# Optimization experiments

Measured on AMD Instinct MI355X. Metric: run time of the kernel, lower is better.

## Reference

```python
import jax, jax.numpy as jnp
import numpy as np

N = 100_000      # nodes
E = 1_600_000    # edges (avg degree 16)
IN, H, OUT = 960, 192, 3
NB = 6           # block_num


def setup_inputs() -> dict:
    key = jax.random.key(0)
    ks = jax.random.split(key, 14)
    s = 0.05  # weight init scale
    x = jax.random.normal(ks[0], (N, IN), jnp.float32)
    src = jax.random.randint(ks[1], (E,), 0, N, jnp.int32)
    dst = jax.random.randint(ks[2], (E,), 0, N, jnp.int32)
    # normalized adjacency values (like D^-1 A entries)
    ew = jax.random.uniform(ks[3], (E,), jnp.float32) / 16.0
    w1 = jax.random.normal(ks[4], (IN, H), jnp.float32) * s
    l1 = jax.random.normal(ks[5], (IN, H), jnp.float32) * s
    b1 = jnp.zeros((H,), jnp.float32)
    wb = jax.random.normal(ks[6], (2 * NB, H, H), jnp.float32) * s
    lb = jax.random.normal(ks[7], (2 * NB, H, H), jnp.float32) * s
    bb = jnp.zeros((2 * NB, H), jnp.float32)
    w2 = jax.random.normal(ks[8], (H, OUT), jnp.float32) * s
    l2 = jax.random.normal(ks[9], (H, OUT), jnp.float32) * s
    b2 = jnp.zeros((OUT,), jnp.float32)
    return dict(x=x, src=src, dst=dst, ew=ew, w1=w1, l1=l1, b1=b1,
                wb=wb, lb=lb, bb=bb, w2=w2, l2=l2, b2=b2)


def reference(x, src, dst, ew, w1, l1, b1, wb, lb, bb, w2, l2, b2):
    def gcn(h, w, lw, b):
        # GraphConvolution: spmm(adj, h @ w) + h @ loop_w + b
        sup = h @ w                                   # [N, F_out]
        msg = sup[src] * ew[:, None]                  # gather + weight  [E, F_out]
        agg = jax.ops.segment_sum(msg, dst, num_segments=N)
        return agg + h @ lw + b

    h = gcn(x, w1, l1, b1)                            # conv1: in_dim -> hidden
    for i in range(NB):                               # GResBlocks
        a = gcn(h, wb[2 * i], lb[2 * i], bb[2 * i])
        a = gcn(a, wb[2 * i + 1], lb[2 * i + 1], bb[2 * i + 1])
        h = (h + a) * 0.5                             # residual scaling
    x_cat = h
    x_out = gcn(x_cat, w2, l2, b2)                    # conv2: hidden -> out_dim
    return (x_out, x_cat)
```

## Files before the change

kernel.cpp:

```cpp
#include <hip/hip_runtime.h>

typedef __attribute__((ext_vector_type(8))) short short8;
typedef __attribute__((ext_vector_type(4))) float f32x4;
typedef __attribute__((ext_vector_type(4))) int int4v;
typedef __attribute__((ext_vector_type(2))) unsigned int u32x2;

__device__ __forceinline__ float bf2f(unsigned short u) {
  return __uint_as_float(((unsigned)u) << 16);
}
__device__ __forceinline__ unsigned short f2bf(float f) {
  unsigned u = __float_as_uint(f);
  return (unsigned short)((u + 0x7FFFu + ((u >> 16) & 1u)) >> 16);
}

#define GLB_CAST(p) ((const __attribute__((address_space(1))) void*)(p))
#define LDS_CAST(p) ((__attribute__((address_space(3))) void*)(p))

__global__ void count_kernel(const int* __restrict__ dst, int* __restrict__ cnt, int E) {
  int e = blockIdx.x * blockDim.x + threadIdx.x;
  if (e < E) atomicAdd(&cnt[dst[e] + 1], 1);
}

__global__ __launch_bounds__(256) void scan_bsum_kernel(const int* __restrict__ cnt,
                                                        int* __restrict__ bsum, int n) {
  __shared__ int buf[256];
  int tid = threadIdx.x;
  int j0 = blockIdx.x * 1024 + tid * 4;
  int s = 0;
#pragma unroll
  for (int k = 0; k < 4; k++) {
    int j = j0 + k;
    if (j < n) s += cnt[j];
  }
  buf[tid] = s;
  __syncthreads();
  for (int off = 128; off > 0; off >>= 1) {
    if (tid < off) buf[tid] += buf[tid + off];
    __syncthreads();
  }
  if (tid == 0) bsum[blockIdx.x] = buf[0];
}

__global__ __launch_bounds__(256) void scan_small_kernel(const int* __restrict__ bsum,
                                                         int* __restrict__ boff, int nb) {
  __shared__ int buf[2][256];
  int tid = threadIdx.x;
  int C = (nb + 255) >> 8;
  int start = tid * C;
  int end = start + C; if (end > nb) end = nb;
  int s = 0;
  for (int j = start; j < end; j++) s += bsum[j];
  buf[0][tid] = s;
  __syncthreads();
  int pin = 0;
  for (int off = 1; off < 256; off <<= 1) {
    int v = buf[pin][tid];
    if (tid >= off) v += buf[pin][tid - off];
    buf[pin ^ 1][tid] = v;
    pin ^= 1;
    __syncthreads();
  }
  int run = (tid == 0) ? 0 : buf[pin][tid - 1];
  for (int j = start; j < end; j++) {
    boff[j] = run;
    run += bsum[j];
  }
}

__global__ __launch_bounds__(256) void scan_final_kernel(const int* __restrict__ cnt,
                                                         const int* __restrict__ boff,
                                                         int* __restrict__ rowptr,
                                                         int* __restrict__ cur,
                                                         int n, int nrows) {
  __shared__ int buf[2][256];
  int tid = threadIdx.x;
  int j0 = blockIdx.x * 1024 + tid * 4;
  int v[4];
  int s = 0;
#pragma unroll
  for (int k = 0; k < 4; k++) {
    int j = j0 + k;
    v[k] = (j < n) ? cnt[j] : 0;
    s += v[k];
  }
  buf[0][tid] = s;
  __syncthreads();
  int pin = 0;
  for (int off = 1; off < 256; off <<= 1) {
    int t = buf[pin][tid];
    if (tid >= off) t += buf[pin][tid - off];
    buf[pin ^ 1][tid] = t;
    pin ^= 1;
    __syncthreads();
  }
  int run = boff[blockIdx.x] + ((tid == 0) ? 0 : buf[pin][tid - 1]);
#pragma unroll
  for (int k = 0; k < 4; k++) {
    int j = j0 + k;
    if (j < n) {
      run += v[k];
      rowptr[j] = run;
      if (j < nrows) cur[j] = run;
    }
  }
}

__global__ void fill_kernel(const int* __restrict__ src, const int* __restrict__ dst,
                            const float* __restrict__ ew,
                            int* __restrict__ cur, int2* __restrict__ s_edge, int E) {
  int e = blockIdx.x * blockDim.x + threadIdx.x;
  if (e >= E) return;
  int r = dst[e];
  int pos = atomicAdd(&cur[r], 1);
  s_edge[pos] = make_int2(src[e], __float_as_int(ew[e]));
}

__global__ void prep_w_kernel(const float* __restrict__ w1,
                              const float* __restrict__ l1,
                              const float* __restrict__ wb,
                              const float* __restrict__ lb,
                              unsigned short* __restrict__ Wt1,
                              unsigned short* __restrict__ Wcatb) {
  int tid = blockIdx.x * blockDim.x + threadIdx.x;
  const int n1 = 30 * 1536 * 8;
  const int nc = 12 * 12 * 768 * 8;
  if (tid < n1) {
    int tile = tid / 12288;
    int r = tid % 12288;
    int slot = r >> 3, e = r & 7;
    int q = slot / 384, c = slot % 384;
    int k = tile * 32 + q * 8 + e;
    Wt1[tid] = f2bf((c < 192) ? w1[k * 192 + c] : l1[k * 192 + (c - 192)]);
  } else if (tid < n1 + nc) {
    int u = tid - n1;
    int i = u / 73728;
    int r = u % 73728;
    int tile = r / 6144;
    int r2 = r % 6144;
    int slot = r2 >> 3, e = r2 & 7;
    int q = slot / 192, c = slot % 192;
    int k = tile * 32 + q * 8 + e;
    Wcatb[u] = f2bf((k < 192) ? wb[((size_t)i * 192 + k) * 192 + c]
                              : lb[((size_t)i * 192 + (k - 192)) * 192 + c]);
  }
}

__device__ __forceinline__ short8 cvt_pair(f32x4 a, f32x4 b) {
  short8 r;
  r[0] = (short)f2bf(a[0]); r[1] = (short)f2bf(a[1]);
  r[2] = (short)f2bf(a[2]); r[3] = (short)f2bf(a[3]);
  r[4] = (short)f2bf(b[0]); r[5] = (short)f2bf(b[1]);
  r[6] = (short)f2bf(b[2]); r[7] = (short)f2bf(b[3]);
  return r;
}

__global__ __launch_bounds__(512) void gemm_f32_kernel(const float* __restrict__ A,
                                                       const unsigned short* __restrict__ Wt,
                                                       unsigned short* __restrict__ out,
                                                       int nrows, int K) {
  __shared__ char lds_raw[40960];

  int tid = threadIdx.x;
  int lane = tid & 63;
  int w = tid >> 6;
  int rg = w >> 1, ch = w & 1;
  int row0blk = blockIdx.x * 256;
  int row0 = row0blk + rg * 64;
  int l15 = lane & 15, lq = lane >> 4;

  f32x4 acc[12][4];
#pragma unroll
  for (int cf = 0; cf < 12; cf++)
#pragma unroll
    for (int rf = 0; rf < 4; rf++) acc[cf][rf] = (f32x4)(0.0f);

  int tiles = K / 32;
  for (int tile = 0; tile < tiles; ++tile) {
    __syncthreads();
#pragma unroll
    for (int it = 0; it < 3; ++it) {
      int slot = it * 512 + tid;
      const unsigned short* g = Wt + ((size_t)tile * 1536 + slot) * 8;
      __builtin_amdgcn_global_load_lds(GLB_CAST(g), LDS_CAST(lds_raw + 16384 + slot * 16), 16, 0, 0);
    }
#pragma unroll
    for (int it = 0; it < 2; ++it) {
      int fs = it * 512 + tid;
      int row = fs >> 2, q8 = fs & 3;
      int grow = row0blk + row;
      if (grow > nrows - 1) grow = nrows - 1;
      const float* g = A + (size_t)grow * K + tile * 32 + q8 * 8;
      f32x4 a0 = *reinterpret_cast<const f32x4*>(g);
      f32x4 a1 = *reinterpret_cast<const f32x4*>(g + 4);
      *reinterpret_cast<short8*>(lds_raw + q8 * 4096 + row * 16) = cvt_pair(a0, a1);
    }
    __syncthreads();

    short8 af[4];
#pragma unroll
    for (int rf = 0; rf < 4; rf++)
      af[rf] = *reinterpret_cast<const short8*>(
          lds_raw + lq * 4096 + (rg * 64 + rf * 16 + l15) * 16);
#pragma unroll
    for (int cf = 0; cf < 12; cf++) {
      const short8 bf = *reinterpret_cast<const short8*>(
          lds_raw + 16384 + (lq * 384 + ch * 192 + cf * 16 + l15) * 16);
#pragma unroll
      for (int rf = 0; rf < 4; rf++)
        acc[cf][rf] = __builtin_amdgcn_mfma_f32_16x16x32_bf16(bf, af[rf], acc[cf][rf], 0, 0, 0);
    }
  }

#pragma unroll
  for (int rf = 0; rf < 4; rf++) {
    int row = row0 + rf * 16 + l15;
    if (row >= nrows) continue;
    unsigned short* orow = out + (size_t)row * 384 + ch * 192 + lq * 4;
#pragma unroll
    for (int cf = 0; cf < 12; cf++) {
      u32x2 pv;
      pv[0] = (unsigned)f2bf(acc[cf][rf][0]) | ((unsigned)f2bf(acc[cf][rf][1]) << 16);
      pv[1] = (unsigned)f2bf(acc[cf][rf][2]) | ((unsigned)f2bf(acc[cf][rf][3]) << 16);
      *reinterpret_cast<u32x2*>(orow + cf * 16) = pv;
    }
  }
}

__global__ __launch_bounds__(256) void spmm_t_kernel(const unsigned short* __restrict__ t,
                                                     const int* __restrict__ rowptr,
                                                     const int2* __restrict__ s_edge,
                                                     const float* __restrict__ bias,
                                                     unsigned short* __restrict__ out16,
                                                     int n) {
  int tid = blockIdx.x * blockDim.x + threadIdx.x;
  int node = tid >> 3;
  int sub = tid & 7;
  if (node >= n) return;
  int co = sub * 8;

  float acc[3][8];
#pragma unroll
  for (int q = 0; q < 3; q++)
#pragma unroll
    for (int j = 0; j < 8; j++) acc[q][j] = 0.0f;

  int e0 = rowptr[node], e1 = rowptr[node + 1];
  int ne = e1 - e0;
  int base = 0;
  for (; base + 8 <= ne; base += 8) {
    int2 rec = s_edge[e0 + base + sub];
#pragma unroll
    for (int half = 0; half < 2; half++) {
      short8 v[4][3];
      float wgt[4];
#pragma unroll
      for (int k = 0; k < 4; k++) {
        int kk = half * 4 + k;
        int sn = __shfl(rec.x, kk, 8);
        wgt[k] = __int_as_float(__shfl(rec.y, kk, 8));
        const unsigned short* row = t + (size_t)sn * 384;
#pragma unroll
        for (int q = 0; q < 3; q++)
          v[k][q] = *reinterpret_cast<const short8*>(row + q * 64 + co);
      }
#pragma unroll
      for (int k = 0; k < 4; k++)
#pragma unroll
        for (int q = 0; q < 3; q++)
#pragma unroll
          for (int j = 0; j < 8; j++)
            acc[q][j] += wgt[k] * bf2f((unsigned short)v[k][q][j]);
    }
  }
  for (; base < ne; base++) {
    int2 rec = s_edge[e0 + base];
    float wgt = __int_as_float(rec.y);
    const unsigned short* row = t + (size_t)rec.x * 384;
#pragma unroll
    for (int q = 0; q < 3; q++) {
      short8 v = *reinterpret_cast<const short8*>(row + q * 64 + co);
#pragma unroll
      for (int j = 0; j < 8; j++) acc[q][j] += wgt * bf2f((unsigned short)v[j]);
    }
  }

  const unsigned short* hlrow = t + (size_t)node * 384 + 192;
#pragma unroll
  for (int q = 0; q < 3; q++) {
    short8 hlv = *reinterpret_cast<const short8*>(hlrow + q * 64 + co);
    unsigned short o16[8];
#pragma unroll
    for (int j = 0; j < 8; j++)
      o16[j] = f2bf(acc[q][j] + bf2f((unsigned short)hlv[j]) + bias[q * 64 + co + j]);
    *reinterpret_cast<int4v*>(&out16[(size_t)node * 192 + q * 64 + co]) =
        *reinterpret_cast<const int4v*>(o16);
  }
}

__global__ __launch_bounds__(256, 3) void fused_res_kernel(const unsigned short* __restrict__ h,
                                                           const int* __restrict__ rowptr,
                                                           const int2* __restrict__ s_edge,
                                                           const unsigned short* __restrict__ Wcat,
                                                           const float* __restrict__ bias,
                                                           const unsigned short* __restrict__ hprev,
                                                           unsigned short* __restrict__ outp,
                                                           int n) {
  extern __shared__ char lds[];
  const int BOFF = 24576;

  int tid = threadIdx.x;
  int lane = tid & 63;
  int row0 = blockIdx.x * 64;
  int rg = tid >> 6;
  int l15 = lane & 15, lq = lane >> 4;

  int myrow = row0 + rg * 16 + l15;
  int myrowc = myrow > n - 1 ? n - 1 : myrow;
  short8 hfrag[6];
#pragma unroll
  for (int t = 0; t < 6; t++)
    hfrag[t] = *reinterpret_cast<const short8*>(h + (size_t)myrowc * 192 + t * 32 + lq * 8);

  {
    int nloc = tid >> 2;
    int sub = tid & 3;
    int grow = row0 + nloc;
    if (grow > n - 1) grow = n - 1;
    float acc[6][8];
#pragma unroll
    for (int jq = 0; jq < 6; jq++)
#pragma unroll
      for (int j = 0; j < 8; j++) acc[jq][j] = 0.0f;

    int e0 = rowptr[grow], e1 = rowptr[grow + 1];
    int ne = e1 - e0;
    int base = 0;
    for (; base + 4 <= ne; base += 4) {
      int2 rec = s_edge[e0 + base + sub];
#pragma unroll
      for (int kp = 0; kp < 2; kp++) {
        short8 v[2][6];
        float wg[2];
#pragma unroll
        for (int k = 0; k < 2; k++) {
          int kk = kp * 2 + k;
          int sn = __shfl(rec.x, kk, 4);
          wg[k] = __int_as_float(__shfl(rec.y, kk, 4));
          const unsigned short* rowp = h + (size_t)sn * 192;
#pragma unroll
          for (int jq = 0; jq < 6; jq++)
            v[k][jq] = *reinterpret_cast<const short8*>(rowp + (jq * 4 + sub) * 8);
        }
#pragma unroll
        for (int k = 0; k < 2; k++)
#pragma unroll
          for (int jq = 0; jq < 6; jq++)
#pragma unroll
            for (int j = 0; j < 8; j++)
              acc[jq][j] += wg[k] * bf2f((unsigned short)v[k][jq][j]);
      }
    }
    for (; base < ne; base++) {
      int2 rec = s_edge[e0 + base];
      float wg = __int_as_float(rec.y);
      const unsigned short* rowp = h + (size_t)rec.x * 192;
#pragma unroll
      for (int jq = 0; jq < 6; jq++) {
        short8 v = *reinterpret_cast<const short8*>(rowp + (jq * 4 + sub) * 8);
#pragma unroll
        for (int j = 0; j < 8; j++) acc[jq][j] += wg * bf2f((unsigned short)v[j]);
      }
    }
#pragma unroll
    for (int jq = 0; jq < 6; jq++) {
      int q = jq * 4 + sub;
      unsigned short o[8];
#pragma unroll
      for (int j = 0; j < 8; j++) o[j] = f2bf(acc[jq][j]);
      *reinterpret_cast<int4v*>(lds + (q * 64 + nloc) * 16) =
          *reinterpret_cast<const int4v*>(o);
    }
  }

  auto stageB = [&](int t, int buf) {
#pragma unroll
    for (int it = 0; it < 3; ++it) {
      int slot = it * 256 + tid;
      const unsigned short* g = Wcat + ((size_t)t * 768 + slot) * 8;
      __builtin_amdgcn_global_load_lds(GLB_CAST(g),
                                       LDS_CAST(lds + BOFF + buf * 12288 + slot * 16), 16, 0, 0);
    }
  };

  stageB(0, 0);
  __syncthreads();

  f32x4 acc[12];
#pragma unroll
  for (int cf = 0; cf < 12; cf++) acc[cf] = (f32x4)(0.0f);

  for (int t = 0; t < 12; ++t) {
    if (t + 1 < 12) stageB(t + 1, (t + 1) & 1);

    short8 af;
    if (t < 6)
      af = *reinterpret_cast<const short8*>(lds + ((t * 4 + lq) * 64 + rg * 16 + l15) * 16);
    else
      af = hfrag[t - 6];

#pragma unroll
    for (int cf = 0; cf < 12; cf++) {
      const short8 bf = *reinterpret_cast<const short8*>(
          lds + BOFF + (t & 1) * 12288 + (lq * 192 + cf * 16 + l15) * 16);
      acc[cf] = __builtin_amdgcn_mfma_f32_16x16x32_bf16(bf, af, acc[cf], 0, 0, 0);
    }
    __syncthreads();
  }

  if (myrow < n) {
    unsigned short* orow = outp + (size_t)myrow * 192 + lq * 4;
#pragma unroll
    for (int cf = 0; cf < 12; cf++) {
      int col = cf * 16 + lq * 4;
      f32x4 bv = *reinterpret_cast<const f32x4*>(bias + col);
      float r[4];
#pragma unroll
      for (int j = 0; j < 4; j++) r[j] = acc[cf][j] + bv[j];
      if (hprev) {
        u32x2 hp = *reinterpret_cast<const u32x2*>(&hprev[(size_t)myrow * 192 + col]);
        r[0] = 0.5f * (bf2f((unsigned short)(hp[0] & 0xFFFF)) + r[0]);
        r[1] = 0.5f * (bf2f((unsigned short)(hp[0] >> 16)) + r[1]);
        r[2] = 0.5f * (bf2f((unsigned short)(hp[1] & 0xFFFF)) + r[2]);
        r[3] = 0.5f * (bf2f((unsigned short)(hp[1] >> 16)) + r[3]);
      }
      u32x2 pv;
      pv[0] = (unsigned)f2bf(r[0]) | ((unsigned)f2bf(r[1]) << 16);
      pv[1] = (unsigned)f2bf(r[2]) | ((unsigned)f2bf(r[3]) << 16);
      *reinterpret_cast<u32x2*>(orow + cf * 16) = pv;
    }
  }
}

__global__ __launch_bounds__(256) void cvt_kernel(const unsigned short* __restrict__ h16,
                                                  float* __restrict__ h32, int n8) {
  int i = blockIdx.x * blockDim.x + threadIdx.x;
  if (i >= n8) return;
  short8 v = *reinterpret_cast<const short8*>(&h16[(size_t)i * 8]);
  f32x4 lo, hi;
#pragma unroll
  for (int j = 0; j < 4; j++) {
    lo[j] = bf2f((unsigned short)v[j]);
    hi[j] = bf2f((unsigned short)v[4 + j]);
  }
  *reinterpret_cast<f32x4*>(&h32[(size_t)i * 8]) = lo;
  *reinterpret_cast<f32x4*>(&h32[(size_t)i * 8 + 4]) = hi;
}

__global__ __launch_bounds__(256) void conv2a_kernel(const unsigned short* __restrict__ h,
                                                     const float* __restrict__ w2,
                                                     const float* __restrict__ l2,
                                                     const float* __restrict__ b2,
                                                     float* __restrict__ sup2,
                                                     float* __restrict__ hl2, int n) {
  int wid = (blockIdx.x * blockDim.x + threadIdx.x) >> 6;
  int lane = threadIdx.x & 63;
  if (wid >= n) return;
  float sa[3] = {0.f, 0.f, 0.f}, sl[3] = {0.f, 0.f, 0.f};
  for (int k = lane; k < 192; k += 64) {
    float hv = bf2f(h[(size_t)wid * 192 + k]);
#pragma unroll
    for (int j = 0; j < 3; j++) {
      sa[j] += hv * w2[k * 3 + j];
      sl[j] += hv * l2[k * 3 + j];
    }
  }
#pragma unroll
  for (int j = 0; j < 3; j++) {
    for (int off = 32; off > 0; off >>= 1) {
      sa[j] += __shfl_down(sa[j], off);
      sl[j] += __shfl_down(sl[j], off);
    }
  }
  if (lane == 0) {
#pragma unroll
    for (int j = 0; j < 3; j++) {
      sup2[(size_t)wid * 3 + j] = sa[j];
      hl2[(size_t)wid * 3 + j] = sl[j] + b2[j];
    }
  }
}

__global__ __launch_bounds__(256) void conv2b_kernel(const int* __restrict__ rowptr,
                                                     const int2* __restrict__ s_edge,
                                                     const float* __restrict__ sup2,
                                                     const float* __restrict__ hl2,
                                                     float* __restrict__ out, int n) {
  int node = blockIdx.x * blockDim.x + threadIdx.x;
  if (node >= n) return;
  float acc[3] = {0.f, 0.f, 0.f};
  int e0 = rowptr[node], e1 = rowptr[node + 1];
  for (int e = e0; e < e1; e++) {
    int2 rec = s_edge[e];
    float wgt = __int_as_float(rec.y);
#pragma unroll
    for (int j = 0; j < 3; j++) acc[j] += wgt * sup2[(size_t)rec.x * 3 + j];
  }
#pragma unroll
  for (int j = 0; j < 3; j++)
    out[(size_t)node * 3 + j] = acc[j] + hl2[(size_t)node * 3 + j];
}

extern "C" void kernel_launch(void* const* d_in, const int* in_sizes, int n_in,
                              void* d_out, int out_size, void* d_ws, size_t ws_size,
                              hipStream_t stream) {
  const float* x  = (const float*)d_in[0];
  const int* src  = (const int*)d_in[1];
  const int* dst  = (const int*)d_in[2];
  const float* ew = (const float*)d_in[3];
  const float* w1 = (const float*)d_in[4];
  const float* l1 = (const float*)d_in[5];
  const float* b1 = (const float*)d_in[6];
  const float* wb = (const float*)d_in[7];
  const float* lb = (const float*)d_in[8];
  const float* bb = (const float*)d_in[9];
  const float* w2 = (const float*)d_in[10];
  const float* l2 = (const float*)d_in[11];
  const float* b2 = (const float*)d_in[12];
  float* out = (float*)d_out;

  const int N = in_sizes[0] / 960;
  const int E = in_sizes[1];

  float* h32 = out + (size_t)N * 3;

  char* p = (char*)d_ws;
  auto alloc = [&](size_t bytes) {
    char* q = p;
    p += (bytes + 255) & ~(size_t)255;
    return q;
  };
  unsigned short* Wt1   = (unsigned short*)alloc((size_t)30 * 1536 * 8 * 2);
  unsigned short* Wcatb = (unsigned short*)alloc((size_t)12 * 12 * 768 * 8 * 2);
  unsigned short* t     = (unsigned short*)alloc((size_t)N * 384 * 2);
  unsigned short* h16a  = (unsigned short*)alloc((size_t)N * 192 * 2);
  unsigned short* h16b  = (unsigned short*)alloc((size_t)N * 192 * 2);
  int* rowptr = (int*)alloc((size_t)(N + 1) * 4);
  int* cur    = (int*)alloc((size_t)N * 4);
  int* cnt    = (int*)alloc((size_t)(N + 1) * 4);
  int* bsum   = (int*)alloc((size_t)1024 * 4);
  int* boff   = (int*)alloc((size_t)1024 * 4);
  int2* s_edge = (int2*)alloc((size_t)E * 8);
  float* sup2 = (float*)alloc((size_t)N * 3 * 4);
  float* hl2  = (float*)alloc((size_t)N * 3 * 4);
  if ((size_t)(p - (char*)d_ws) > ws_size) return;

  unsigned short* a16 = t;

  const int nScan = N + 1;
  const int nBlk = (nScan + 1023) / 1024;

  hipMemsetAsync(cnt, 0, (size_t)(N + 1) * 4, stream);
  count_kernel<<<(E + 255) / 256, 256, 0, stream>>>(dst, cnt, E);
  scan_bsum_kernel<<<nBlk, 256, 0, stream>>>(cnt, bsum, nScan);
  scan_small_kernel<<<1, 256, 0, stream>>>(bsum, boff, nBlk);
  scan_final_kernel<<<nBlk, 256, 0, stream>>>(cnt, boff, rowptr, cur, nScan, N);
  fill_kernel<<<(E + 255) / 256, 256, 0, stream>>>(src, dst, ew, cur, s_edge, E);
  {
    int total = 30 * 1536 * 8 + 12 * 12 * 768 * 8;
    prep_w_kernel<<<(total + 255) / 256, 256, 0, stream>>>(w1, l1, wb, lb, Wt1, Wcatb);
  }

  int gBlocks = (N + 255) / 256;
  int sBlocks = (N * 8 + 255) / 256;
  int fBlocks = (N + 63) / 64;
  const int F_LDS = 49152;

  gemm_f32_kernel<<<gBlocks, 512, 0, stream>>>(x, Wt1, t, N, 960);
  spmm_t_kernel<<<sBlocks, 256, 0, stream>>>(t, rowptr, s_edge, b1, h16a, N);

  unsigned short* hcur = h16a;
  unsigned short* hnxt = h16b;
  for (int i = 0; i < 12; i += 2) {
    fused_res_kernel<<<fBlocks, 256, F_LDS, stream>>>(
        hcur, rowptr, s_edge, Wcatb + (size_t)i * 73728, bb + (size_t)i * 192,
        (const unsigned short*)nullptr, a16, N);
    fused_res_kernel<<<fBlocks, 256, F_LDS, stream>>>(
        a16, rowptr, s_edge, Wcatb + (size_t)(i + 1) * 73728, bb + (size_t)(i + 1) * 192,
        hcur, hnxt, N);
    unsigned short* tmp = hcur; hcur = hnxt; hnxt = tmp;
  }

  cvt_kernel<<<(N * 24 + 255) / 256, 256, 0, stream>>>(hcur, h32, N * 24);

  conv2a_kernel<<<(N + 3) / 4, 256, 0, stream>>>(hcur, w2, l2, b2, sup2, hl2, N);
  conv2b_kernel<<<(N + 255) / 256, 256, 0, stream>>>(rowptr, s_edge, sup2, hl2, out, N);
}
```

Measured before the change: 2.152 ms.

## Shrink fused residual kernel tile to 32 rows and split output columns across waves

The fused SpMM+GEMM residual kernel now processes 32 nodes per block instead of 64. Each node's gather uses 8 threads with 3 chunks instead of 4 threads with 6 chunks, which halves the per-thread accumulator registers. In the MFMA phase, waves split the 192 output columns into two halves, so each wave holds 6 accumulators instead of 12. LDS drops to 36KB and launch bounds rise to 4 blocks per SM to raise occupancy and latency hiding for the gather. The cost is that each 192x384 weight tile is now staged once per 32 rows rather than per 64, doubling weight traffic from L2 into LDS.

```diff
diff --git a/kernel.cpp b/kernel.cpp
--- a/kernel.cpp
+++ b/kernel.cpp
@@ -297,7 +297,7 @@
   }
 }
 
-__global__ __launch_bounds__(256, 3) void fused_res_kernel(const unsigned short* __restrict__ h,
+__global__ __launch_bounds__(256, 4) void fused_res_kernel(const unsigned short* __restrict__ h,
                                                            const int* __restrict__ rowptr,
                                                            const int2* __restrict__ s_edge,
                                                            const unsigned short* __restrict__ Wcat,
@@ -306,81 +306,83 @@
                                                            unsigned short* __restrict__ outp,
                                                            int n) {
   extern __shared__ char lds[];
-  const int BOFF = 24576;
+  const int BOFF = 12288;
 
   int tid = threadIdx.x;
   int lane = tid & 63;
-  int row0 = blockIdx.x * 64;
-  int rg = tid >> 6;
-  int l15 = lane & 15, lq = lane >> 4;
-
-  int myrow = row0 + rg * 16 + l15;
-  int myrowc = myrow > n - 1 ? n - 1 : myrow;
-  short8 hfrag[6];
-#pragma unroll
-  for (int t = 0; t < 6; t++)
-    hfrag[t] = *reinterpret_cast<const short8*>(h + (size_t)myrowc * 192 + t * 32 + lq * 8);
+  int row0 = blockIdx.x * 32;
 
   {
-    int nloc = tid >> 2;
-    int sub = tid & 3;
+    int nloc = tid >> 3;
+    int sub = tid & 7;
+    int co = sub * 8;
     int grow = row0 + nloc;
     if (grow > n - 1) grow = n - 1;
-    float acc[6][8];
-#pragma unroll
-    for (int jq = 0; jq < 6; jq++)
-#pragma unroll
-      for (int j = 0; j < 8; j++) acc[jq][j] = 0.0f;
+    float acc[3][8];
+#pragma unroll
+    for (int q = 0; q < 3; q++)
+#pragma unroll
+      for (int j = 0; j < 8; j++) acc[q][j] = 0.0f;
 
     int e0 = rowptr[grow], e1 = rowptr[grow + 1];
     int ne = e1 - e0;
     int base = 0;
-    for (; base + 4 <= ne; base += 4) {
+    for (; base + 8 <= ne; base += 8) {
       int2 rec = s_edge[e0 + base + sub];
 #pragma unroll
-      for (int kp = 0; kp < 2; kp++) {
-        short8 v[2][6];
-        float wg[2];
-#pragma unroll
-        for (int k = 0; k < 2; k++) {
-          int kk = kp * 2 + k;
-          int sn = __shfl(rec.x, kk, 4);
-          wg[k] = __int_as_float(__shfl(rec.y, kk, 4));
+      for (int half = 0; half < 2; half++) {
+        short8 v[4][3];
+        float wgt[4];
+#pragma unroll
+        for (int k = 0; k < 4; k++) {
+          int kk = half * 4 + k;
+          int sn = __shfl(rec.x, kk, 8);
+          wgt[k] = __int_as_float(__shfl(rec.y, kk, 8));
           const unsigned short* rowp = h + (size_t)sn * 192;
 #pragma unroll
-          for (int jq = 0; jq < 6; jq++)
-            v[k][jq] = *reinterpret_cast<const short8*>(rowp + (jq * 4 + sub) * 8);
+          for (int q = 0; q < 3; q++)
+            v[k][q] = *reinterpret_cast<const short8*>(rowp + q * 64 + co);
         }
 #pragma unroll
-        for (int k = 0; k < 2; k++)
-#pragma unroll
-          for (int jq = 0; jq < 6; jq++)
+        for (int k = 0; k < 4; k++)
+#pragma unroll
+          for (int q = 0; q < 3; q++)
 #pragma unroll
             for (int j = 0; j < 8; j++)
-              acc[jq][j] += wg[k] * bf2f((unsigned short)v[k][jq][j]);
+              acc[q][j] += wgt[k] * bf2f((unsigned short)v[k][q][j]);
       }
     }
     for (; base < ne; base++) {
       int2 rec = s_edge[e0 + base];
-      float wg = __int_as_float(rec.y);
+      float wgt = __int_as_float(rec.y);
       const unsigned short* rowp = h + (size_t)rec.x * 192;
 #pragma unroll
-      for (int jq = 0; jq < 6; jq++) {
-        short8 v = *reinterpret_cast<const short8*>(rowp + (jq * 4 + sub) * 8);
-#pragma unroll
-        for (int j = 0; j < 8; j++) acc[jq][j] += wg * bf2f((unsigned short)v[j]);
+      for (int q = 0; q < 3; q++) {
+        short8 v = *reinterpret_cast<const short8*>(rowp + q * 64 + co);
+#pragma unroll
+        for (int j = 0; j < 8; j++) acc[q][j] += wgt * bf2f((unsigned short)v[j]);
       }
     }
 #pragma unroll
-    for (int jq = 0; jq < 6; jq++) {
-      int q = jq * 4 + sub;
+    for (int q = 0; q < 3; q++) {
       unsigned short o[8];
 #pragma unroll
-      for (int j = 0; j < 8; j++) o[j] = f2bf(acc[jq][j]);
-      *reinterpret_cast<int4v*>(lds + (q * 64 + nloc) * 16) =
+      for (int j = 0; j < 8; j++) o[j] = f2bf(acc[q][j]);
+      *reinterpret_cast<int4v*>(lds + ((q * 8 + sub) * 32 + nloc) * 16) =
           *reinterpret_cast<const int4v*>(o);
     }
   }
+
+  int rg = (tid >> 6) & 1;
+  int ch = tid >> 7;
+  int l15 = lane & 15, lq = lane >> 4;
+  int myrow = row0 + rg * 16 + l15;
+  int myrowc = myrow > n - 1 ? n - 1 : myrow;
+
+  short8 hfrag[6];
+#pragma unroll
+  for (int t = 0; t < 6; t++)
+    hfrag[t] = *reinterpret_cast<const short8*>(h + (size_t)myrowc * 192 + t * 32 + lq * 8);
 
   auto stageB = [&](int t, int buf) {
 #pragma unroll
@@ -395,33 +397,33 @@
   stageB(0, 0);
   __syncthreads();
 
-  f32x4 acc[12];
-#pragma unroll
-  for (int cf = 0; cf < 12; cf++) acc[cf] = (f32x4)(0.0f);
+  f32x4 acc[6];
+#pragma unroll
+  for (int cf = 0; cf < 6; cf++) acc[cf] = (f32x4)(0.0f);
 
   for (int t = 0; t < 12; ++t) {
     if (t + 1 < 12) stageB(t + 1, (t + 1) & 1);
 
     short8 af;
     if (t < 6)
-      af = *reinterpret_cast<const short8*>(lds + ((t * 4 + lq) * 64 + rg * 16 + l15) * 16);
+      af = *reinterpret_cast<const short8*>(lds + ((t * 4 + lq) * 32 + rg * 16 + l15) * 16);
     else
       af = hfrag[t - 6];
 
 #pragma unroll
-    for (int cf = 0; cf < 12; cf++) {
+    for (int cf = 0; cf < 6; cf++) {
       const short8 bf = *reinterpret_cast<const short8*>(
-          lds + BOFF + (t & 1) * 12288 + (lq * 192 + cf * 16 + l15) * 16);
+          lds + BOFF + (t & 1) * 12288 + (lq * 192 + ch * 96 + cf * 16 + l15) * 16);
       acc[cf] = __builtin_amdgcn_mfma_f32_16x16x32_bf16(bf, af, acc[cf], 0, 0, 0);
     }
     __syncthreads();
   }
 
   if (myrow < n) {
-    unsigned short* orow = outp + (size_t)myrow * 192 + lq * 4;
-#pragma unroll
-    for (int cf = 0; cf < 12; cf++) {
-      int col = cf * 16 + lq * 4;
+    unsigned short* orow = outp + (size_t)myrow * 192 + ch * 96 + lq * 4;
+#pragma unroll
+    for (int cf = 0; cf < 6; cf++) {
+      int col = ch * 96 + cf * 16 + lq * 4;
       f32x4 bv = *reinterpret_cast<const f32x4*>(bias + col);
       float r[4];
 #pragma unroll
@@ -572,8 +574,8 @@
 
   int gBlocks = (N + 255) / 256;
   int sBlocks = (N * 8 + 255) / 256;
-  int fBlocks = (N + 63) / 64;
-  const int F_LDS = 49152;
+  int fBlocks = (N + 31) / 32;
+  const int F_LDS = 36864;
 
   gemm_f32_kernel<<<gBlocks, 512, 0, stream>>>(x, Wt1, t, N, 960);
   spmm_t_kernel<<<sBlocks, 256, 0, stream>>>(t, rowptr, s_edge, b1, h16a, N);
```

After: 3.231 ms. +50.1%, slower.
